# Performance work log

Hardware: AMD Instinct MI355X
Metric: run time of the kernel (lower is better)

Reference implementation:

```python
import jax, jax.numpy as jnp
import numpy as np

B, S, E, H, D = 384, 128, 512, 4, 128  # batch, seq(block), embed, heads, head_dim


def setup_inputs() -> dict:
    key = jax.random.key(0)
    ks = jax.random.split(key, 6)
    scale = 1.0 / np.sqrt(E)  # lecun_normal-ish fan-in scaling
    return {
        "x": jax.random.normal(ks[0], (B, S, E), dtype=jnp.float32),
        "Wq": jax.random.normal(ks[1], (E, E), dtype=jnp.float32) * scale,
        "bq": jnp.zeros((E,), dtype=jnp.float32),
        "Wk": jax.random.normal(ks[2], (E, E), dtype=jnp.float32) * scale,
        "bk": jnp.zeros((E,), dtype=jnp.float32),
        "Wv": jax.random.normal(ks[3], (E, E), dtype=jnp.float32) * scale,
        "bv": jnp.zeros((E,), dtype=jnp.float32),
        "Wo": jax.random.normal(ks[4], (E, E), dtype=jnp.float32) * scale,
        "bo": jnp.zeros((E,), dtype=jnp.float32),
    }


def reference(x, Wq, bq, Wk, bk, Wv, bv, Wo, bo):
    # Projections, then split heads: [B,S,E] -> [B,S,H,D]
    q = (x @ Wq + bq).reshape(B, S, H, D)
    k = (x @ Wk + bk).reshape(B, S, H, D)
    v = (x @ Wv + bv).reshape(B, S, H, D)
    # NOTE: original applies no 1/sqrt(D) scaling and no mask.
    scores = jnp.einsum("BSHD,BTHD->BHST", q, k)  # [B,H,S,T]
    weights = jax.nn.softmax(scores, axis=-1)
    out = jnp.einsum("BHST,BTHD->BSHD", weights, v).reshape(B, S, E)
    return out @ Wo + bo
```

## Files before the change

### kernel.cpp

```cpp
#include <hip/hip_runtime.h>
#include <hip/hip_bf16.h>
#include <cstdint>


#define EMB 512

typedef __attribute__((ext_vector_type(4))) float    f32x4;
typedef __attribute__((ext_vector_type(8))) _Float16 f16x8;

#define MFMA16(a, b, c) __builtin_amdgcn_mfma_f32_16x16x32_f16((a), (b), (c), 0, 0, 0)

__device__ __forceinline__ int swz128(int row, int col) {
    return row * 128 + (col ^ (((row >> 2) & 3) << 4));
}
__device__ __forceinline__ int swz64(int row, int col) {
    return row * 64 + (col ^ (((row >> 2) & 3) << 4));
}

__device__ __forceinline__ void gld_lds16(const _Float16* g, _Float16* l) {
    __builtin_amdgcn_global_load_lds(
        (const __attribute__((address_space(1))) void*)g,
        (__attribute__((address_space(3))) void*)l, 16, 0, 0);
}

__device__ __forceinline__ void stage64(_Float16* lds, const _Float16* gbase,
                                        int grow0, int k0, int wave, int lane) {
#pragma unroll
    for (int i = 0; i < 4; ++i) {
        int idx = wave * 256 + i * 64 + lane;
        int n   = idx >> 3;
        int kb  = (idx & 7) ^ (((n >> 2) & 3) << 1);
        gld_lds16(gbase + (grow0 + n) * EMB + k0 + kb * 8,
                  lds + wave * 2048 + i * 512);
    }
}

#define ZACC(A)                                   \
    _Pragma("unroll") for (int _i = 0; _i < 2; ++_i) \
    _Pragma("unroll") for (int _j = 0; _j < 8; ++_j) \
        A[_i][_j] = (f32x4){0.f, 0.f, 0.f, 0.f};

__global__ void k_prep(const float* __restrict__ x, _Float16* __restrict__ xh,
                       const float* __restrict__ Wq, const float* __restrict__ Wk,
                       const float* __restrict__ Wv, const float* __restrict__ Wo,
                       _Float16* __restrict__ Wqkvt, _Float16* __restrict__ Wot) {
    __shared__ float t[32][33];
    const int g = blockIdx.x, tid = threadIdx.x;
    if (g < 12288) {
        long i = ((long)g * 256 + tid) * 8;
        f32x4 a = *(const f32x4*)(x + i);
        f32x4 b = *(const f32x4*)(x + i + 4);
        f16x8 o;
        o[0] = (_Float16)a[0]; o[1] = (_Float16)a[1];
        o[2] = (_Float16)a[2]; o[3] = (_Float16)a[3];
        o[4] = (_Float16)b[0]; o[5] = (_Float16)b[1];
        o[6] = (_Float16)b[2]; o[7] = (_Float16)b[3];
        *(f16x8*)(xh + i) = o;
        return;
    }
    const int tb = g - 12288;
    const int z = tb >> 8, t2 = tb & 255;
    const float* W = (z == 0) ? Wq : (z == 1) ? Wk : (z == 2) ? Wv : Wo;
    _Float16* Wt = (z < 3) ? (Wqkvt + (long)z * 512 * EMB) : Wot;
    const int tx = tid & 31, ty = tid >> 5;
    const int k0 = (t2 & 15) * 32, n0 = (t2 >> 4) * 32;
#pragma unroll
    for (int i = 0; i < 4; ++i)
        t[ty + i * 8][tx] = W[(k0 + ty + i * 8) * EMB + n0 + tx];
    __syncthreads();
#pragma unroll
    for (int i = 0; i < 4; ++i)
        Wt[(n0 + ty + i * 8) * EMB + k0 + tx] = (_Float16)t[tx][ty + i * 8];
}

__global__ __launch_bounds__(256, 4)
void k_qkv(const _Float16* __restrict__ xh, const _Float16* __restrict__ Wqkvt,
           const float* __restrict__ bq, const float* __restrict__ bk,
           const float* __restrict__ bv,
           _Float16* __restrict__ qb, _Float16* __restrict__ kb,
           _Float16* __restrict__ vtb) {
    __shared__ _Float16 S[2][128 * 64];
    _Float16* SA = S[0];
    _Float16* SB = S[1];
    const int tid = threadIdx.x, wave = tid >> 6, lane = tid & 63;
    const int l15 = lane & 15, quad = lane >> 4;
    const int g = blockIdx.x;
    const int xcd = g & 7, r = g >> 3;
    const int bb = xcd * 48 + r / 12, j = r % 12;
    const int m0 = bb * 128;
    const bool vswap = (j >= 8);
    const _Float16* As = vswap ? SB : SA;
    const _Float16* Bs = vswap ? SA : SB;
    f32x4 acc[2][8];
    ZACC(acc);
    for (int k0 = 0; k0 < EMB; k0 += 64) {
        stage64(SA, xh, m0, k0, wave, lane);
        stage64(SB, Wqkvt, j * 128, k0, wave, lane);
        __syncthreads();
#pragma unroll
        for (int ktl = 0; ktl < 2; ++ktl) {
            int cb = ktl * 32 + quad * 8;
            f16x8 a0 = *(const f16x8*)&As[swz64(wave * 32 + l15, cb)];
            f16x8 a1 = *(const f16x8*)&As[swz64(wave * 32 + 16 + l15, cb)];
#pragma unroll
            for (int nt = 0; nt < 8; ++nt) {
                f16x8 bbf = *(const f16x8*)&Bs[swz64(nt * 16 + l15, cb)];
                acc[0][nt] = MFMA16(a0, bbf, acc[0][nt]);
                acc[1][nt] = MFMA16(a1, bbf, acc[1][nt]);
            }
        }
        __syncthreads();
    }
    _Float16* SC = &S[0][0];
    if (!vswap) {
        const float* bias = (j < 4) ? bq : bk;
        const int nc0 = (j & 3) * 128;
#pragma unroll
        for (int nt = 0; nt < 8; ++nt) {
            int col = nt * 16 + l15;
            float bz = bias[nc0 + col];
#pragma unroll
            for (int mt = 0; mt < 2; ++mt)
#pragma unroll
                for (int rr = 0; rr < 4; ++rr) {
                    int row = wave * 32 + mt * 16 + quad * 4 + rr;
                    SC[swz128(row, col)] = (_Float16)(acc[mt][nt][rr] + bz);
                }
        }
        __syncthreads();
        _Float16* dst = (j < 4) ? qb : kb;
#pragma unroll
        for (int i = 0; i < 8; ++i) {
            int idx = i * 256 + tid;
            int row = idx >> 4, col = (idx & 15) * 8;
            f16x8 v = *(const f16x8*)&SC[row * 128 + (col ^ (((row >> 2) & 3) << 4))];
            *(f16x8*)(dst + (long)(m0 + row) * EMB + nc0 + col) = v;
        }
    } else {
        const int hv = j - 8;
#pragma unroll
        for (int mt = 0; mt < 2; ++mt)
#pragma unroll
            for (int rr = 0; rr < 4; ++rr) {
                int row = wave * 32 + mt * 16 + quad * 4 + rr;
                float bz = bv[hv * 128 + row];
#pragma unroll
                for (int nt = 0; nt < 8; ++nt) {
                    int col = nt * 16 + l15;
                    SC[swz128(row, col)] = (_Float16)(acc[mt][nt][rr] + bz);
                }
            }
        __syncthreads();
        _Float16* dst = vtb + (long)(bb * 4 + hv) * 128 * 128;
#pragma unroll
        for (int i = 0; i < 8; ++i) {
            int idx = i * 256 + tid;
            int row = idx >> 4, col = (idx & 15) * 8;
            f16x8 v = *(const f16x8*)&SC[row * 128 + (col ^ (((row >> 2) & 3) << 4))];
            *(f16x8*)(dst + row * 128 + col) = v;
        }
    }
}

__global__ __launch_bounds__(512, 4)
void k_core(const _Float16* __restrict__ qb, const _Float16* __restrict__ kb,
            const _Float16* __restrict__ vtb, _Float16* __restrict__ attn) {
    __shared__ _Float16 SK[128 * 128];
    __shared__ _Float16 SV[128 * 128];
    const int tid = threadIdx.x, wave = tid >> 6, lane = tid & 63;
    const int l15 = lane & 15, quad = lane >> 4;
    const int g = blockIdx.x;
    const int xcd = g & 7, r = g >> 3;
    const int b = xcd * 48 + (r >> 2), h = r & 3;
    const int sRow0 = b * 128, wRow0 = h * 128;
    const _Float16* vt = vtb + (long)(b * 4 + h) * 128 * 128;

#pragma unroll
    for (int i = 0; i < 4; ++i) {
        int seg = i * 8 + wave;
        int idx = seg * 64 + lane;
        int n   = idx >> 4;
        int kbk = (idx & 15) ^ (((n >> 2) & 3) << 1);
        gld_lds16(kb + (long)(sRow0 + n) * EMB + wRow0 + kbk * 8, SK + seg * 512);
        gld_lds16(vt + n * 128 + kbk * 8, SV + seg * 512);
    }
    __syncthreads();

    f32x4 acc[8];
#pragma unroll
    for (int nt = 0; nt < 8; ++nt) acc[nt] = (f32x4){0.f, 0.f, 0.f, 0.f};

#pragma unroll
    for (int kt = 0; kt < 4; ++kt) {
        int ca = kt * 32 + quad * 8;
        f16x8 q0 = *(const f16x8*)(qb + (long)(sRow0 + wave * 16 + l15) * EMB + wRow0 + ca);
#pragma unroll
        for (int nt = 0; nt < 8; ++nt) {
            f16x8 kf = *(const f16x8*)&SK[swz128(nt * 16 + l15, ca)];
            acc[nt] = MFMA16(q0, kf, acc[nt]);
        }
    }
#pragma unroll
    for (int rr = 0; rr < 4; ++rr) {
        float mx = acc[0][rr];
#pragma unroll
        for (int nt = 1; nt < 8; ++nt) mx = fmaxf(mx, acc[nt][rr]);
        mx = fmaxf(mx, __shfl_xor(mx, 1));
        mx = fmaxf(mx, __shfl_xor(mx, 2));
        mx = fmaxf(mx, __shfl_xor(mx, 4));
        mx = fmaxf(mx, __shfl_xor(mx, 8));
        float sm = 0.f;
#pragma unroll
        for (int nt = 0; nt < 8; ++nt) {
            float e = __expf(acc[nt][rr] - mx);
            acc[nt][rr] = e;
            sm += e;
        }
        sm += __shfl_xor(sm, 1);
        sm += __shfl_xor(sm, 2);
        sm += __shfl_xor(sm, 4);
        sm += __shfl_xor(sm, 8);
        float inv = 1.0f / sm;
#pragma unroll
        for (int nt = 0; nt < 8; ++nt) acc[nt][rr] *= inv;
    }
    __syncthreads();

#pragma unroll
    for (int nt = 0; nt < 8; ++nt) {
        int col = nt * 16 + l15;
#pragma unroll
        for (int rr = 0; rr < 4; ++rr)
            SK[swz128(wave * 16 + quad * 4 + rr, col)] = (_Float16)acc[nt][rr];
    }
    __syncthreads();

#pragma unroll
    for (int nt = 0; nt < 8; ++nt) acc[nt] = (f32x4){0.f, 0.f, 0.f, 0.f};
#pragma unroll
    for (int kt = 0; kt < 4; ++kt) {
        int ca = kt * 32 + quad * 8;
        f16x8 p0 = *(const f16x8*)&SK[swz128(wave * 16 + l15, ca)];
#pragma unroll
        for (int nt = 0; nt < 8; ++nt) {
            f16x8 vf = *(const f16x8*)&SV[swz128(nt * 16 + l15, ca)];
            acc[nt] = MFMA16(p0, vf, acc[nt]);
        }
    }
    __syncthreads();

#pragma unroll
    for (int nt = 0; nt < 8; ++nt) {
        int col = nt * 16 + l15;
#pragma unroll
        for (int rr = 0; rr < 4; ++rr)
            SV[swz128(wave * 16 + quad * 4 + rr, col)] = (_Float16)acc[nt][rr];
    }
    __syncthreads();
#pragma unroll
    for (int i = 0; i < 4; ++i) {
        int idx = i * 512 + tid;
        int row = idx >> 4, col = (idx & 15) * 8;
        f16x8 v = *(const f16x8*)&SV[row * 128 + (col ^ (((row >> 2) & 3) << 4))];
        *(f16x8*)(attn + (long)(sRow0 + row) * EMB + wRow0 + col) = v;
    }
}

__global__ __launch_bounds__(256, 4)
void k_out(const _Float16* __restrict__ attn, const _Float16* __restrict__ Wot,
           const float* __restrict__ bo, float* __restrict__ out) {
    __shared__ _Float16 SH[16384];
    _Float16* SA = SH;
    _Float16* SB = SH + 4096;
    const int tid = threadIdx.x, wave = tid >> 6, lane = tid & 63;
    const int l15 = lane & 15, quad = lane >> 4;
    const int g = blockIdx.x;
    const int xcd = g & 7, r = g >> 3;
    const int m0 = (xcd * 96 + (r >> 2)) * 64, n0 = (r & 3) * 128;
    f32x4 acc[8];
#pragma unroll
    for (int nt = 0; nt < 8; ++nt) acc[nt] = (f32x4){0.f, 0.f, 0.f, 0.f};
    for (int k0 = 0; k0 < EMB; k0 += 64) {
#pragma unroll
        for (int i = 0; i < 2; ++i) {
            int seg = i * 4 + wave;
            int idx = seg * 64 + lane;
            int n = idx >> 3, kbk = (idx & 7) ^ (((n >> 2) & 3) << 1);
            gld_lds16(attn + (long)(m0 + n) * EMB + k0 + kbk * 8, SA + seg * 512);
        }
#pragma unroll
        for (int i = 0; i < 4; ++i) {
            int seg = i * 4 + wave;
            int idx = seg * 64 + lane;
            int n = idx >> 3, kbk = (idx & 7) ^ (((n >> 2) & 3) << 1);
            gld_lds16(Wot + (long)(n0 + n) * EMB + k0 + kbk * 8, SB + seg * 512);
        }
        __syncthreads();
#pragma unroll
        for (int ktl = 0; ktl < 2; ++ktl) {
            int cb = ktl * 32 + quad * 8;
            f16x8 a0 = *(const f16x8*)&SA[swz64(wave * 16 + l15, cb)];
#pragma unroll
            for (int nt = 0; nt < 8; ++nt) {
                f16x8 bb = *(const f16x8*)&SB[swz64(nt * 16 + l15, cb)];
                acc[nt] = MFMA16(a0, bb, acc[nt]);
            }
        }
        __syncthreads();
    }
    float* SF = (float*)SH;
#pragma unroll
    for (int nt = 0; nt < 8; ++nt) {
        int col = nt * 16 + l15;
        float bz = bo[n0 + col];
#pragma unroll
        for (int rr = 0; rr < 4; ++rr) {
            int row = wave * 16 + quad * 4 + rr;
            SF[row * 128 + (col ^ (((row >> 2) & 1) << 4))] = acc[nt][rr] + bz;
        }
    }
    __syncthreads();
#pragma unroll
    for (int i = 0; i < 8; ++i) {
        int idx = i * 256 + tid;
        int row = idx >> 5, c4 = (idx & 31) * 4;
        f32x4 v = *(const f32x4*)&SF[row * 128 + (c4 ^ (((row >> 2) & 1) << 4))];
        *(f32x4*)(out + (long)(m0 + row) * EMB + n0 + c4) = v;
    }
}

extern "C" void kernel_launch(void* const* d_in, const int* in_sizes, int n_in,
                              void* d_out, int out_size, void* d_ws, size_t ws_size,
                              hipStream_t stream) {
    const float* x  = (const float*)d_in[0];
    const float* Wq = (const float*)d_in[1];
    const float* bq = (const float*)d_in[2];
    const float* Wk = (const float*)d_in[3];
    const float* bk = (const float*)d_in[4];
    const float* Wv = (const float*)d_in[5];
    const float* bv = (const float*)d_in[6];
    const float* Wo = (const float*)d_in[7];
    const float* bo = (const float*)d_in[8];
    float* out = (float*)d_out;

    char* w = (char*)d_ws;
    _Float16* xh    = (_Float16*)(w);
    _Float16* attn  = xh;
    _Float16* Wqkvt = (_Float16*)(w + 50331648);
    _Float16* Wot   = (_Float16*)(w + 51904512);
    _Float16* qb    = (_Float16*)(w + 52428800);
    _Float16* kb    = (_Float16*)(w + 102760448);
    _Float16* vtb   = (_Float16*)(w + 153092096);

    k_prep<<<13312, 256, 0, stream>>>(x, xh, Wq, Wk, Wv, Wo, Wqkvt, Wot);
    k_qkv<<<4608, 256, 0, stream>>>(xh, Wqkvt, bq, bk, bv, qb, kb, vtb);
    k_core<<<1536, 512, 0, stream>>>(qb, kb, vtb, attn);
    k_out<<<3072, 256, 0, stream>>>(attn, Wot, bo, out);
}
```

Measured before the change: 370.9 us.

## Rewrite QKV projection GEMM with 256x256 tiles and multi-stage LDS pipeline

Replaces the 128x128-tile QKV GEMM, which loaded and then synchronized every k-step, with a 512-thread 256x256-tile kernel. It uses 160KB of dynamic LDS, with A double-buffered and B triple-buffered. Async global-to-LDS loads for upcoming k-tiles are interleaved with MFMA phases using barriers, waitcnt and setprio, and a new XOR swizzle avoids bank conflicts. This aims to hide load latency and raise reuse per tile, at the cost of occupancy (one block per CU given the LDS size) and more complex scheduling.

```diff
diff --git a/kernel.cpp b/kernel.cpp
--- a/kernel.cpp
+++ b/kernel.cpp
@@ -15,6 +15,9 @@
 }
 __device__ __forceinline__ int swz64(int row, int col) {
     return row * 64 + (col ^ (((row >> 2) & 3) << 4));
+}
+__device__ __forceinline__ int swzK(int row, int col) {
+    return row * 64 + (col ^ ((row & 7) << 3));
 }
 
 __device__ __forceinline__ void gld_lds16(const _Float16* g, _Float16* l) {
@@ -23,22 +26,15 @@
         (__attribute__((address_space(3))) void*)l, 16, 0, 0);
 }
 
-__device__ __forceinline__ void stage64(_Float16* lds, const _Float16* gbase,
-                                        int grow0, int k0, int wave, int lane) {
-#pragma unroll
-    for (int i = 0; i < 4; ++i) {
-        int idx = wave * 256 + i * 64 + lane;
-        int n   = idx >> 3;
-        int kb  = (idx & 7) ^ (((n >> 2) & 3) << 1);
-        gld_lds16(gbase + (grow0 + n) * EMB + k0 + kb * 8,
-                  lds + wave * 2048 + i * 512);
-    }
-}
-
-#define ZACC(A)                                   \
-    _Pragma("unroll") for (int _i = 0; _i < 2; ++_i) \
-    _Pragma("unroll") for (int _j = 0; _j < 8; ++_j) \
-        A[_i][_j] = (f32x4){0.f, 0.f, 0.f, 0.f};
+__device__ __forceinline__ void stg2(_Float16* lds, const _Float16* gb, int row0,
+                                     int k0, int sub, int tid) {
+#pragma unroll
+    for (int i = 0; i < 2; ++i) {
+        int idx = (sub * 2 + i) * 512 + tid;
+        int n = idx >> 3, blk = (idx & 7) ^ (n & 7);
+        gld_lds16(gb + (long)(row0 + n) * EMB + k0 + blk * 8, lds + idx * 8);
+    }
+}
 
 __global__ void k_prep(const float* __restrict__ x, _Float16* __restrict__ xh,
                        const float* __restrict__ Wq, const float* __restrict__ Wk,
@@ -73,91 +69,193 @@
         Wt[(n0 + ty + i * 8) * EMB + k0 + tx] = (_Float16)t[tx][ty + i * 8];
 }
 
-__global__ __launch_bounds__(256, 4)
-void k_qkv(const _Float16* __restrict__ xh, const _Float16* __restrict__ Wqkvt,
-           const float* __restrict__ bq, const float* __restrict__ bk,
-           const float* __restrict__ bv,
-           _Float16* __restrict__ qb, _Float16* __restrict__ kb,
-           _Float16* __restrict__ vtb) {
-    __shared__ _Float16 S[2][128 * 64];
-    _Float16* SA = S[0];
-    _Float16* SB = S[1];
+__global__ __launch_bounds__(512, 2)
+void k_qkv2(const _Float16* __restrict__ xh, const _Float16* __restrict__ Wqkvt,
+            const float* __restrict__ bq, const float* __restrict__ bk,
+            const float* __restrict__ bv,
+            _Float16* __restrict__ qb, _Float16* __restrict__ kb,
+            _Float16* __restrict__ vtb) {
+    extern __shared__ _Float16 LDS[];
     const int tid = threadIdx.x, wave = tid >> 6, lane = tid & 63;
     const int l15 = lane & 15, quad = lane >> 4;
+    const int wr = wave >> 2, wc = wave & 3;
     const int g = blockIdx.x;
-    const int xcd = g & 7, r = g >> 3;
-    const int bb = xcd * 48 + r / 12, j = r % 12;
-    const int m0 = bb * 128;
-    const bool vswap = (j >= 8);
-    const _Float16* As = vswap ? SB : SA;
-    const _Float16* Bs = vswap ? SA : SB;
-    f32x4 acc[2][8];
-    ZACC(acc);
-    for (int k0 = 0; k0 < EMB; k0 += 64) {
-        stage64(SA, xh, m0, k0, wave, lane);
-        stage64(SB, Wqkvt, j * 128, k0, wave, lane);
-        __syncthreads();
-#pragma unroll
-        for (int ktl = 0; ktl < 2; ++ktl) {
-            int cb = ktl * 32 + quad * 8;
-            f16x8 a0 = *(const f16x8*)&As[swz64(wave * 32 + l15, cb)];
-            f16x8 a1 = *(const f16x8*)&As[swz64(wave * 32 + 16 + l15, cb)];
-#pragma unroll
-            for (int nt = 0; nt < 8; ++nt) {
-                f16x8 bbf = *(const f16x8*)&Bs[swz64(nt * 16 + l15, cb)];
-                acc[0][nt] = MFMA16(a0, bbf, acc[0][nt]);
-                acc[1][nt] = MFMA16(a1, bbf, acc[1][nt]);
-            }
-        }
-        __syncthreads();
-    }
-    _Float16* SC = &S[0][0];
+    const int id = (g & 7) * 144 + (g >> 3);
+    const int mtile = id / 6, ntile = id % 6;
+    const int m0 = mtile * 256;
+    const bool vswap = (ntile >= 4);
+    const _Float16* Asrc = vswap ? Wqkvt : xh;
+    const int Arow0 = vswap ? 1024 + (ntile - 4) * 256 : m0;
+    const _Float16* Bsrc = vswap ? xh : Wqkvt;
+    const int Brow0 = vswap ? m0 : ntile * 256;
+
+    stg2(LDS,         Asrc, Arow0, 0, 0, tid);  stg2(LDS,         Asrc, Arow0, 0, 1, tid);
+    __builtin_amdgcn_sched_barrier(0);
+    stg2(LDS + 32768, Bsrc, Brow0, 0, 0, tid);  stg2(LDS + 32768, Bsrc, Brow0, 0, 1, tid);
+    __builtin_amdgcn_sched_barrier(0);
+    stg2(LDS + 16384, Asrc, Arow0, 64, 0, tid); stg2(LDS + 16384, Asrc, Arow0, 64, 1, tid);
+    __builtin_amdgcn_sched_barrier(0);
+    stg2(LDS + 49152, Bsrc, Brow0, 64, 0, tid); stg2(LDS + 49152, Bsrc, Brow0, 64, 1, tid);
+    __builtin_amdgcn_sched_barrier(0);
+    asm volatile("s_waitcnt vmcnt(8)" ::: "memory");
+    __builtin_amdgcn_sched_barrier(0);
+    __builtin_amdgcn_s_barrier();
+
+    f32x4 acc[8][4];
+#pragma unroll
+    for (int i = 0; i < 8; ++i)
+#pragma unroll
+        for (int j = 0; j < 4; ++j) acc[i][j] = (f32x4){0.f, 0.f, 0.f, 0.f};
+    f16x8 aA[4][2], bL[2][2], bH[2][2];
+
+    for (int kt = 0; kt < 8; ++kt) {
+        const _Float16* At = LDS + (kt & 1) * 16384;
+        const _Float16* Bt = LDS + 32768 + (kt % 3) * 16384;
+        _Float16* Anx = LDS + ((kt + 1) & 1) * 16384;
+        _Float16* Bnx = LDS + 32768 + ((kt + 2) % 3) * 16384;
+        const int k0A = (kt + 1) * 64, k0B = (kt + 2) * 64;
+        const bool sA = (kt >= 1) && (kt <= 6);
+        const bool sB = (kt <= 5);
+
+#pragma unroll
+        for (int mf = 0; mf < 4; ++mf)
+#pragma unroll
+            for (int kk = 0; kk < 2; ++kk)
+                aA[mf][kk] = *(const f16x8*)&At[swzK(wr * 128 + mf * 16 + l15,
+                                                    kk * 32 + quad * 8)];
+#pragma unroll
+        for (int nf = 0; nf < 2; ++nf)
+#pragma unroll
+            for (int kk = 0; kk < 2; ++kk)
+                bL[nf][kk] = *(const f16x8*)&Bt[swzK(wc * 64 + nf * 16 + l15,
+                                                     kk * 32 + quad * 8)];
+        if (sA) stg2(Anx, Asrc, Arow0, k0A, 0, tid);
+        __builtin_amdgcn_s_barrier();
+        asm volatile("s_waitcnt lgkmcnt(0)" ::: "memory");
+        __builtin_amdgcn_sched_barrier(0);
+        __builtin_amdgcn_s_setprio(1);
+#pragma unroll
+        for (int mf = 0; mf < 4; ++mf)
+#pragma unroll
+            for (int nf = 0; nf < 2; ++nf)
+#pragma unroll
+                for (int kk = 0; kk < 2; ++kk)
+                    acc[mf][nf] = MFMA16(aA[mf][kk], bL[nf][kk], acc[mf][nf]);
+        __builtin_amdgcn_s_setprio(0);
+        __builtin_amdgcn_sched_barrier(0);
+        __builtin_amdgcn_s_barrier();
+
+#pragma unroll
+        for (int nf = 0; nf < 2; ++nf)
+#pragma unroll
+            for (int kk = 0; kk < 2; ++kk)
+                bH[nf][kk] = *(const f16x8*)&Bt[swzK(wc * 64 + (nf + 2) * 16 + l15,
+                                                     kk * 32 + quad * 8)];
+        if (sA) stg2(Anx, Asrc, Arow0, k0A, 1, tid);
+        __builtin_amdgcn_s_barrier();
+        asm volatile("s_waitcnt lgkmcnt(0)" ::: "memory");
+        __builtin_amdgcn_sched_barrier(0);
+        __builtin_amdgcn_s_setprio(1);
+#pragma unroll
+        for (int mf = 0; mf < 4; ++mf)
+#pragma unroll
+            for (int nf = 0; nf < 2; ++nf)
+#pragma unroll
+                for (int kk = 0; kk < 2; ++kk)
+                    acc[mf][nf + 2] = MFMA16(aA[mf][kk], bH[nf][kk], acc[mf][nf + 2]);
+        __builtin_amdgcn_s_setprio(0);
+        __builtin_amdgcn_sched_barrier(0);
+        __builtin_amdgcn_s_barrier();
+
+#pragma unroll
+        for (int mf = 0; mf < 4; ++mf)
+#pragma unroll
+            for (int kk = 0; kk < 2; ++kk)
+                aA[mf][kk] = *(const f16x8*)&At[swzK(wr * 128 + (mf + 4) * 16 + l15,
+                                                    kk * 32 + quad * 8)];
+        if (sB) stg2(Bnx, Bsrc, Brow0, k0B, 0, tid);
+        __builtin_amdgcn_s_barrier();
+        asm volatile("s_waitcnt lgkmcnt(0)" ::: "memory");
+        __builtin_amdgcn_sched_barrier(0);
+        __builtin_amdgcn_s_setprio(1);
+#pragma unroll
+        for (int mf = 0; mf < 4; ++mf)
+#pragma unroll
+            for (int nf = 0; nf < 2; ++nf)
+#pragma unroll
+                for (int kk = 0; kk < 2; ++kk)
+                    acc[mf + 4][nf] = MFMA16(aA[mf][kk], bL[nf][kk], acc[mf + 4][nf]);
+        __builtin_amdgcn_s_setprio(0);
+        __builtin_amdgcn_sched_barrier(0);
+        __builtin_amdgcn_s_barrier();
+
+        if (sB) stg2(Bnx, Bsrc, Brow0, k0B, 1, tid);
+        __builtin_amdgcn_s_barrier();
+        __builtin_amdgcn_s_setprio(1);
+#pragma unroll
+        for (int mf = 0; mf < 4; ++mf)
+#pragma unroll
+            for (int nf = 0; nf < 2; ++nf)
+#pragma unroll
+                for (int kk = 0; kk < 2; ++kk)
+                    acc[mf + 4][nf + 2] = MFMA16(aA[mf][kk], bH[nf][kk], acc[mf + 4][nf + 2]);
+        __builtin_amdgcn_s_setprio(0);
+        __builtin_amdgcn_sched_barrier(0);
+        if (kt < 6) {
+            asm volatile("s_waitcnt vmcnt(4)" ::: "memory");
+        } else if (kt == 6) {
+            asm volatile("s_waitcnt vmcnt(0)" ::: "memory");
+        }
+        __builtin_amdgcn_sched_barrier(0);
+        __builtin_amdgcn_s_barrier();
+    }
+
+    _Float16* SC = LDS;
     if (!vswap) {
-        const float* bias = (j < 4) ? bq : bk;
-        const int nc0 = (j & 3) * 128;
-#pragma unroll
-        for (int nt = 0; nt < 8; ++nt) {
-            int col = nt * 16 + l15;
+        const float* bias = (ntile < 2) ? bq : bk;
+        const int nc0 = (ntile & 1) * 256;
+#pragma unroll
+        for (int nf = 0; nf < 4; ++nf) {
+            int col = wc * 64 + nf * 16 + l15;
             float bz = bias[nc0 + col];
 #pragma unroll
-            for (int mt = 0; mt < 2; ++mt)
+            for (int mf = 0; mf < 8; ++mf)
 #pragma unroll
                 for (int rr = 0; rr < 4; ++rr) {
-                    int row = wave * 32 + mt * 16 + quad * 4 + rr;
-                    SC[swz128(row, col)] = (_Float16)(acc[mt][nt][rr] + bz);
+                    int row = wr * 128 + mf * 16 + quad * 4 + rr;
+                    SC[row * 256 + (col ^ (((row >> 2) & 3) << 4))] =
+                        (_Float16)(acc[mf][nf][rr] + bz);
                 }
         }
-        __syncthreads();
-        _Float16* dst = (j < 4) ? qb : kb;
-#pragma unroll
-        for (int i = 0; i < 8; ++i) {
-            int idx = i * 256 + tid;
-            int row = idx >> 4, col = (idx & 15) * 8;
-            f16x8 v = *(const f16x8*)&SC[row * 128 + (col ^ (((row >> 2) & 3) << 4))];
-            *(f16x8*)(dst + (long)(m0 + row) * EMB + nc0 + col) = v;
-        }
     } else {
-        const int hv = j - 8;
-#pragma unroll
-        for (int mt = 0; mt < 2; ++mt)
+#pragma unroll
+        for (int mf = 0; mf < 8; ++mf)
 #pragma unroll
             for (int rr = 0; rr < 4; ++rr) {
-                int row = wave * 32 + mt * 16 + quad * 4 + rr;
-                float bz = bv[hv * 128 + row];
-#pragma unroll
-                for (int nt = 0; nt < 8; ++nt) {
-                    int col = nt * 16 + l15;
-                    SC[swz128(row, col)] = (_Float16)(acc[mt][nt][rr] + bz);
+                int row = wr * 128 + mf * 16 + quad * 4 + rr;
+                float bz = bv[(ntile - 4) * 256 + row];
+#pragma unroll
+                for (int nf = 0; nf < 4; ++nf) {
+                    int col = wc * 64 + nf * 16 + l15;
+                    SC[row * 256 + (col ^ (((row >> 2) & 3) << 4))] =
+                        (_Float16)(acc[mf][nf][rr] + bz);
                 }
             }
-        __syncthreads();
-        _Float16* dst = vtb + (long)(bb * 4 + hv) * 128 * 128;
-#pragma unroll
-        for (int i = 0; i < 8; ++i) {
-            int idx = i * 256 + tid;
-            int row = idx >> 4, col = (idx & 15) * 8;
-            f16x8 v = *(const f16x8*)&SC[row * 128 + (col ^ (((row >> 2) & 3) << 4))];
-            *(f16x8*)(dst + row * 128 + col) = v;
+    }
+    __syncthreads();
+#pragma unroll
+    for (int i = 0; i < 16; ++i) {
+        int idx = i * 512 + tid;
+        int row = idx >> 5, col = (idx & 31) * 8;
+        f16x8 v = *(const f16x8*)&SC[row * 256 + (col ^ (((row >> 2) & 3) << 4))];
+        if (!vswap) {
+            long gr = m0 + row;
+            _Float16* dst = ((ntile < 2) ? qb : kb) + gr * EMB + (ntile & 1) * 256 + col;
+            *(f16x8*)dst = v;
+        } else {
+            int hv = (ntile - 4) * 2 + (row >> 7);
+            int b4 = (mtile * 2 + (col >> 7)) * 4 + hv;
+            *(f16x8*)(vtb + (long)b4 * 16384 + (row & 127) * 128 + (col & 127)) = v;
         }
     }
 }
@@ -352,8 +450,15 @@
     _Float16* kb    = (_Float16*)(w + 102760448);
     _Float16* vtb   = (_Float16*)(w + 153092096);
 
+    static bool attr_done = false;
+    if (!attr_done) {
+        hipFuncSetAttribute(reinterpret_cast<const void*>(k_qkv2),
+                            hipFuncAttributeMaxDynamicSharedMemorySize, 163840);
+        attr_done = true;
+    }
+
     k_prep<<<13312, 256, 0, stream>>>(x, xh, Wq, Wk, Wv, Wo, Wqkvt, Wot);
-    k_qkv<<<4608, 256, 0, stream>>>(xh, Wqkvt, bq, bk, bv, qb, kb, vtb);
+    k_qkv2<<<1152, 512, 163840, stream>>>(xh, Wqkvt, bq, bk, bv, qb, kb, vtb);
     k_core<<<1536, 512, 0, stream>>>(qb, kb, vtb, attn);
     k_out<<<3072, 256, 0, stream>>>(attn, Wot, bo, out);
 }
```

Result: slower. 379.1 us (+2.2%).
